# Kernel tuning notes

Measured on AMD Instinct MI355X. Metric: run time of the kernel, lower is better.

The kernel has to match this reference:

```python
import jax, jax.numpy as jnp
import numpy as np

D_MODEL = 1024
N_HEADS = 16
D_K = D_MODEL // N_HEADS
LN_EPS = 1e-5


def setup_inputs() -> dict:
    key = jax.random.key(0)
    ks = jax.random.split(key, 10)
    s = 1.0 / np.sqrt(D_MODEL)
    x = jax.random.normal(ks[0], (8, 1024, D_MODEL), dtype=jnp.float32)
    return {
        "x": x,
        "Wq": jax.random.uniform(ks[1], (D_MODEL, D_MODEL), jnp.float32, -s, s),
        "bq": jax.random.uniform(ks[2], (D_MODEL,), jnp.float32, -s, s),
        "Wk": jax.random.uniform(ks[3], (D_MODEL, D_MODEL), jnp.float32, -s, s),
        "bk": jax.random.uniform(ks[4], (D_MODEL,), jnp.float32, -s, s),
        "Wv": jax.random.uniform(ks[5], (D_MODEL, D_MODEL), jnp.float32, -s, s),
        "bv": jax.random.uniform(ks[6], (D_MODEL,), jnp.float32, -s, s),
        "Wo": jax.random.uniform(ks[7], (D_MODEL, D_MODEL), jnp.float32, -s, s),
        "bo": jax.random.uniform(ks[8], (D_MODEL,), jnp.float32, -s, s),
        "gamma": jnp.ones((D_MODEL,), jnp.float32),
        "beta": jnp.zeros((D_MODEL,), jnp.float32),
    }


def reference(x, Wq, bq, Wk, bk, Wv, bv, Wo, bo, gamma, beta):
    B, S, D = x.shape
    H, dk = N_HEADS, D_K
    # projections -> [B, H, S, dk]
    q = (x @ Wq.T + bq).reshape(B, S, H, dk).transpose(0, 2, 1, 3)
    k = (x @ Wk.T + bk).reshape(B, S, H, dk).transpose(0, 2, 1, 3)
    v = (x @ Wv.T + bv).reshape(B, S, H, dk).transpose(0, 2, 1, 3)
    scores = jnp.einsum('bhqd,bhkd->bhqk', q, k) / jnp.sqrt(jnp.float32(dk))
    attn = jax.nn.softmax(scores, axis=-1)  # dropout: eval mode (identity)
    ctx = jnp.einsum('bhqk,bhkd->bhqd', attn, v)
    ctx = ctx.transpose(0, 2, 1, 3).reshape(B, S, D)
    out = ctx @ Wo.T + bo
    h = out + x  # residual
    mu = jnp.mean(h, axis=-1, keepdims=True)
    var = jnp.mean((h - mu) ** 2, axis=-1, keepdims=True)
    y = (h - mu) * jax.lax.rsqrt(var + LN_EPS) * gamma + beta
    return y, attn
```

## Files before the change

kernel.cpp:

```cpp
#include <hip/hip_runtime.h>
#include <math.h>

#define D 1024
#define H 16
#define DK 64
#define SQ 1024
#define NB 8
#define NROW (NB*SQ)

typedef __attribute__((ext_vector_type(8))) short bf16x8;
typedef __attribute__((ext_vector_type(4))) float f32x4;

__device__ __forceinline__ ushort f2bf(float x){
    unsigned u = __builtin_bit_cast(unsigned, x);
    u += 0x7FFFu + ((u >> 16) & 1u);
    return (ushort)(u >> 16);
}
__device__ __forceinline__ float bf2f(ushort u){
    return __builtin_bit_cast(float, (unsigned)u << 16);
}

__device__ __forceinline__ f32x4 mfma16(bf16x8 a, bf16x8 b, f32x4 c){
    return __builtin_amdgcn_mfma_f32_16x16x32_bf16(a, b, c, 0, 0, 0);
}

__device__ __forceinline__ void gload16(const void* g, void* l){
    __builtin_amdgcn_global_load_lds(
        (const __attribute__((address_space(1))) unsigned int*)g,
        (__attribute__((address_space(3))) unsigned int*)l, 16, 0, 0);
}

__device__ __forceinline__ bf16x8 gld8(const ushort* p){
    return __builtin_bit_cast(bf16x8, *(const uint4*)p);
}

__global__ __launch_bounds__(256)
void cvt_all(const float* __restrict__ x,
             const float* __restrict__ Wq, const float* __restrict__ Wk,
             const float* __restrict__ Wv, const float* __restrict__ Wo,
             ushort* __restrict__ xb, ushort* __restrict__ wb_)
{
    const int bid = blockIdx.x;
    const float* s; ushort* d; size_t off;
    if (bid < 4096) { s = x; d = xb; off = (size_t)bid * 2048; }
    else {
        int r = bid - 4096;
        int wsel = r >> 9;
        if      (wsel == 0) s = Wq;
        else if (wsel == 1) s = Wk;
        else if (wsel == 2) s = Wv;
        else                s = Wo;
        d = wb_ + (size_t)wsel * 1048576;
        off = (size_t)(r & 511) * 2048;
    }
    size_t i = off + (size_t)threadIdx.x * 8;
    float4 a = *(const float4*)(s + i);
    float4 b = *(const float4*)(s + i + 4);
    ushort tmp[8] = {f2bf(a.x),f2bf(a.y),f2bf(a.z),f2bf(a.w),
                     f2bf(b.x),f2bf(b.y),f2bf(b.z),f2bf(b.w)};
    *(uint4*)(d + i) = *(uint4*)tmp;
}

__device__ __forceinline__ void stage_g(const ushort* __restrict__ g, int ldg,
                                        ushort* lds, int t)
{
#pragma unroll
    for (int i = 0; i < 2; ++i){
        int c = i*256 + t;
        int row = c >> 2, sc = c & 3;
        int gch = sc ^ (row & 3);
        gload16(g + (size_t)row*ldg + gch*8, lds + c*8);
    }
}
__device__ __forceinline__ bf16x8 gfrag(const ushort* lds, int row, int kc)
{
    uint4 v = ((const uint4*)lds)[row*4 + (kc ^ (row & 3))];
    return __builtin_bit_cast(bf16x8, v);
}

__global__ __launch_bounds__(256)
void gemm_qkv(const ushort* __restrict__ A, const ushort* __restrict__ Wp,
              const float* __restrict__ bq, const float* __restrict__ bk,
              const float* __restrict__ bv,
              ushort* __restrict__ Qb, ushort* __restrict__ Kb,
              ushort* __restrict__ Vtb)
{
    __shared__ ushort As[4096];
    __shared__ ushort Bs[4096];
    const int t = threadIdx.x, lane = t & 63, w = t >> 6;
    const int wr = w >> 1, wc = w & 1, lr = lane & 15, kg = lane >> 4;
    const int bx = blockIdx.x % 24, by = blockIdx.x / 24;
    const int i0 = by * 128, j0 = bx * 128;
    const int section = bx >> 3;
    const ushort* Ab = A  + (size_t)i0 * 1024;
    const ushort* Wb = Wp + (size_t)j0 * 1024;
    const float* bias = (section == 0) ? bq : (section == 1) ? bk : bv;
    ushort* outp      = (section == 0) ? Qb : (section == 1) ? Kb : Vtb;

    f32x4 acc[4][4];
#pragma unroll
    for (int m = 0; m < 4; ++m)
#pragma unroll
        for (int n = 0; n < 4; ++n) acc[m][n] = (f32x4){0.f,0.f,0.f,0.f};

    for (int k0 = 0; k0 < 1024; k0 += 32){
        __syncthreads();
        stage_g(Ab + k0, 1024, As, t);
        stage_g(Wb + k0, 1024, Bs, t);
        __syncthreads();
        bf16x8 af[4], bfr[4];
#pragma unroll
        for (int m = 0; m < 4; ++m) af[m]  = gfrag(As, wr*64 + m*16 + lr, kg);
#pragma unroll
        for (int n = 0; n < 4; ++n) bfr[n] = gfrag(Bs, wc*64 + n*16 + lr, kg);
#pragma unroll
        for (int m = 0; m < 4; ++m)
#pragma unroll
            for (int n = 0; n < 4; ++n)
                acc[m][n] = mfma16(af[m], bfr[n], acc[m][n]);
    }

#pragma unroll
    for (int m = 0; m < 4; ++m){
        int rt = i0 + wr*64 + m*16 + kg*4;
#pragma unroll
        for (int n = 0; n < 4; ++n){
            int jc = ((j0 + wc*64 + n*16 + lr) & 1023);
            float bj = bias[jc];
            int hh = jc >> 6, dd = jc & 63;
#pragma unroll
            for (int j = 0; j < 4; ++j){
                int i = rt + j;
                int b = i >> 10, s = i & 1023;
                float v = acc[m][n][j] + bj;
                size_t idx = (section < 2)
                    ? ((((size_t)b*H + hh)*SQ + s)*DK + dd)
                    : ((((size_t)b*H + hh)*DK + dd)*SQ + s);
                outp[idx] = f2bf(v);
            }
        }
    }
}

__global__ __launch_bounds__(256)
void gemm_o(const ushort* __restrict__ A, const ushort* __restrict__ W,
            const float* __restrict__ bias, const float* __restrict__ resid,
            float* __restrict__ out)
{
    __shared__ ushort As[4096];
    __shared__ ushort Bs[4096];
    const int t = threadIdx.x, lane = t & 63, w = t >> 6;
    const int wr = w >> 1, wc = w & 1, lr = lane & 15, kg = lane >> 4;
    const int i0 = blockIdx.y * 128, j0 = blockIdx.x * 128;
    const ushort* Ab = A + (size_t)i0 * 1024;
    const ushort* Wb = W + (size_t)j0 * 1024;

    f32x4 acc[4][4];
#pragma unroll
    for (int m = 0; m < 4; ++m)
#pragma unroll
        for (int n = 0; n < 4; ++n) acc[m][n] = (f32x4){0.f,0.f,0.f,0.f};

    for (int k0 = 0; k0 < 1024; k0 += 32){
        __syncthreads();
        stage_g(Ab + k0, 1024, As, t);
        stage_g(Wb + k0, 1024, Bs, t);
        __syncthreads();
        bf16x8 af[4], bfr[4];
#pragma unroll
        for (int m = 0; m < 4; ++m) af[m]  = gfrag(As, wr*64 + m*16 + lr, kg);
#pragma unroll
        for (int n = 0; n < 4; ++n) bfr[n] = gfrag(Bs, wc*64 + n*16 + lr, kg);
#pragma unroll
        for (int m = 0; m < 4; ++m)
#pragma unroll
            for (int n = 0; n < 4; ++n)
                acc[m][n] = mfma16(af[m], bfr[n], acc[m][n]);
    }

#pragma unroll
    for (int m = 0; m < 4; ++m){
        int rt = i0 + wr*64 + m*16 + kg*4;
#pragma unroll
        for (int n = 0; n < 4; ++n){
            int ct = j0 + wc*64 + n*16 + lr;
            float bj = bias[ct];
#pragma unroll
            for (int j = 0; j < 4; ++j){
                int i = rt + j;
                out[(size_t)i*1024 + ct] = acc[m][n][j] + bj + resid[(size_t)i*1024 + ct];
            }
        }
    }
}

__device__ __forceinline__ void stage64x64(const ushort* __restrict__ g, int ldg,
                                           ushort* lds, int t)
{
#pragma unroll
    for (int i = 0; i < 2; ++i){
        int c = i*256 + t;
        int row = c >> 3, sc = c & 7;
        int gch = sc ^ (row & 7);
        gload16(g + (size_t)row*ldg + gch*8, lds + c*8);
    }
}
__device__ __forceinline__ bf16x8 frag_ld(const ushort* lds, int row, int chunk)
{
    uint4 v = ((const uint4*)lds)[row*8 + (chunk ^ (row & 7))];
    return __builtin_bit_cast(bf16x8, v);
}

__global__ __launch_bounds__(256)
void attn_v10(const ushort* __restrict__ Q, const ushort* __restrict__ K,
              const ushort* __restrict__ Vt, float* __restrict__ attn_out,
              ushort* __restrict__ ctx)
{
    __shared__ ushort KV[2][8192];
    __shared__ ushort Ps[4][1024];

    const int t    = threadIdx.x;
    const int lane = t & 63;
    const int w    = t >> 6;
    const int lr   = lane & 15, kg = lane >> 4;
    const int bid  = blockIdx.x;
    const int qt   = bid >> 7, bh = bid & 127;
    const int b    = bh >> 4, hh = bh & 15;
    const size_t base = (size_t)bh * SQ * DK;

    bf16x8 qf[2];
    {
        const ushort* qrow = Q + base + (size_t)(qt*64 + w*16 + lr) * DK + kg*8;
        qf[0] = gld8(qrow);
        qf[1] = gld8(qrow + 32);
    }

    const float CEXP = 0.18033688011112042f;

    float lsum[4] = {0.f, 0.f, 0.f, 0.f};
    stage64x64(K + base, DK, KV[0], t);
    for (int kt = 0; kt < 16; ++kt) {
        const int cur = kt & 1;
        __syncthreads();
        if (kt < 15)
            stage64x64(K + base + (size_t)(kt+1)*64*DK, DK, KV[cur^1], t);
        const ushort* Ks = KV[cur];
#pragma unroll
        for (int n = 0; n < 4; ++n) {
            f32x4 z = {0.f,0.f,0.f,0.f};
            z = mfma16(qf[0], frag_ld(Ks, n*16+lr, kg),   z);
            z = mfma16(qf[1], frag_ld(Ks, n*16+lr, 4+kg), z);
#pragma unroll
            for (int r = 0; r < 4; ++r)
                lsum[r] += exp2f(z[r] * CEXP);
        }
    }
    float invl[4];
#pragma unroll
    for (int r = 0; r < 4; ++r) {
        float s = lsum[r];
#pragma unroll
        for (int msk = 1; msk < 16; msk <<= 1) s += __shfl_xor(s, msk, 64);
        invl[r] = 1.0f / s;
    }

    f32x4 acc_o[4];
#pragma unroll
    for (int n = 0; n < 4; ++n) acc_o[n] = (f32x4){0.f,0.f,0.f,0.f};

    float* ap0 = attn_out + ((size_t)bh*SQ + (size_t)qt*64 + w*16)*SQ;
    ushort* pw = &Ps[w][0];

    stage64x64(K  + base, DK, KV[0],        t);
    stage64x64(Vt + base, SQ, KV[0] + 4096, t);
    asm volatile("s_waitcnt vmcnt(0) lgkmcnt(0)" ::: "memory");
    __builtin_amdgcn_s_barrier();
    __builtin_amdgcn_sched_barrier(0);

    for (int kt = 0; kt < 16; ++kt) {
        const int cur = kt & 1;
        if (kt < 15) {
            stage64x64(K  + base + (size_t)(kt+1)*64*DK, DK, KV[cur^1],        t);
            stage64x64(Vt + base + (size_t)(kt+1)*64,    SQ, KV[cur^1] + 4096, t);
        }
        const ushort* Ks = KV[cur];
        const ushort* Vs = KV[cur] + 4096;

        f32x4 sc[4];
#pragma unroll
        for (int n = 0; n < 4; ++n) {
            f32x4 z = {0.f,0.f,0.f,0.f};
            z = mfma16(qf[0], frag_ld(Ks, n*16+lr, kg),   z);
            z = mfma16(qf[1], frag_ld(Ks, n*16+lr, 4+kg), z);
            sc[n] = z;
        }
#pragma unroll
        for (int n = 0; n < 4; ++n) {
#pragma unroll
            for (int r = 0; r < 4; ++r) {
                float p = exp2f(sc[n][r] * CEXP) * invl[r];
                int row = kg*4 + r, col = n*16 + lr;
                pw[row*64 + ((col>>3) ^ (row&7))*8 + (col&7)] = f2bf(p);
            }
        }
        bf16x8 a0 = frag_ld(pw, lr, kg);
        bf16x8 a1 = frag_ld(pw, lr, 4+kg);
#pragma unroll
        for (int n = 0; n < 4; ++n) {
            acc_o[n] = mfma16(a0, frag_ld(Vs, n*16+lr, kg),   acc_o[n]);
            acc_o[n] = mfma16(a1, frag_ld(Vs, n*16+lr, 4+kg), acc_o[n]);
        }
#pragma unroll
        for (int rr = 0; rr < 4; ++rr) {
            int row = kg*4 + rr;
            int cidx = row*64 + ((lr>>1) ^ (row&7))*8 + (lr&1)*4;
            uint2 pk = *(const uint2*)(pw + cidx);
            float4 o;
            o.x = bf2f((ushort)(pk.x & 0xFFFF));
            o.y = bf2f((ushort)(pk.x >> 16));
            o.z = bf2f((ushort)(pk.y & 0xFFFF));
            o.w = bf2f((ushort)(pk.y >> 16));
            *(float4*)(ap0 + (size_t)row*SQ + kt*64 + lr*4) = o;
        }
        if (kt < 15) {
            asm volatile("s_waitcnt vmcnt(4) lgkmcnt(0)" ::: "memory");
            __builtin_amdgcn_s_barrier();
            __builtin_amdgcn_sched_barrier(0);
        }
    }

    ushort* cp = ctx + ((size_t)b*SQ + (size_t)qt*64 + w*16)*D + hh*DK;
#pragma unroll
    for (int n = 0; n < 4; ++n)
#pragma unroll
        for (int r = 0; r < 4; ++r)
            cp[(size_t)(kg*4+r)*D + n*16 + lr] = f2bf(acc_o[n][r]);
}

__global__ __launch_bounds__(256)
void ln_k(const float* __restrict__ hbuf, const float* __restrict__ gamma,
          const float* __restrict__ beta, float* __restrict__ y)
{
    const int row = blockIdx.x, t = threadIdx.x;
    float4 v = ((const float4*)(hbuf + (size_t)row * D))[t];
    float s  = v.x + v.y + v.z + v.w;
    float sq = v.x*v.x + v.y*v.y + v.z*v.z + v.w*v.w;
#pragma unroll
    for (int o = 32; o >= 1; o >>= 1) {
        s  += __shfl_down(s, o, 64);
        sq += __shfl_down(sq, o, 64);
    }
    __shared__ float rs_[4], rq_[4], mu_s, rstd_s;
    int wid = t >> 6;
    if ((t & 63) == 0) { rs_[wid] = s; rq_[wid] = sq; }
    __syncthreads();
    if (t == 0) {
        float S  = rs_[0]+rs_[1]+rs_[2]+rs_[3];
        float Q2 = rq_[0]+rq_[1]+rq_[2]+rq_[3];
        float mu  = S * (1.0f/1024.0f);
        float var = Q2 * (1.0f/1024.0f) - mu*mu;
        mu_s = mu; rstd_s = rsqrtf(var + 1e-5f);
    }
    __syncthreads();
    float mu = mu_s, rstd = rstd_s;
    float4 g = ((const float4*)gamma)[t];
    float4 be = ((const float4*)beta)[t];
    float4 o;
    o.x = (v.x-mu)*rstd*g.x + be.x;
    o.y = (v.y-mu)*rstd*g.y + be.y;
    o.z = (v.z-mu)*rstd*g.z + be.z;
    o.w = (v.w-mu)*rstd*g.w + be.w;
    ((float4*)(y + (size_t)row * D))[t] = o;
}

extern "C" void kernel_launch(void* const* d_in, const int* in_sizes, int n_in,
                              void* d_out, int out_size, void* d_ws, size_t ws_size,
                              hipStream_t stream)
{
    const float* x     = (const float*)d_in[0];
    const float* Wq    = (const float*)d_in[1];
    const float* bq    = (const float*)d_in[2];
    const float* Wk    = (const float*)d_in[3];
    const float* bk    = (const float*)d_in[4];
    const float* Wv    = (const float*)d_in[5];
    const float* bv    = (const float*)d_in[6];
    const float* Wo    = (const float*)d_in[7];
    const float* bo    = (const float*)d_in[8];
    const float* gamma = (const float*)d_in[9];
    const float* beta  = (const float*)d_in[10];

    float* y    = (float*)d_out;
    float* attn = (float*)d_out + (size_t)NROW * D;

    const size_t SZ  = (size_t)NROW * D;
    const size_t WSZ = (size_t)D * D;
    ushort* ws   = (ushort*)d_ws;
    ushort* xb   = ws;
    ushort* Wpk  = xb  + SZ;
    ushort* Wob  = Wpk + 3*WSZ;
    ushort* Qb   = Wob + WSZ;
    ushort* Kb   = Qb  + SZ;
    ushort* Vtb  = Kb  + SZ;
    ushort* Cb   = Vtb + SZ;
    float*  Hb   = (float*)(Cb + SZ);

    cvt_all<<<6144, 256, 0, stream>>>(x, Wq, Wk, Wv, Wo, xb, Wpk);

    gemm_qkv<<<1536, 256, 0, stream>>>(xb, Wpk, bq, bk, bv, Qb, Kb, Vtb);

    attn_v10<<<2048, 256, 0, stream>>>(Qb, Kb, Vtb, attn, Cb);

    gemm_o<<<dim3(8, 64), 256, 0, stream>>>(Cb, Wob, bo, x, Hb);

    ln_k<<<NROW, 256, 0, stream>>>(Hb, gamma, beta, y);
}
```

Measured before the change: 334.5 us.

## Double K-tile depth in projection GEMMs and swizzle block order for L2 reuse

The QKV and output-projection GEMMs now stage 64-wide K slices instead of 32, using the 8-chunk XOR-swizzled LDS layout. This halves the number of barrier pairs per tile and puts twice as many MFMAs between syncs. Block indices are also remapped with an XCD-aware swizzle so that neighbouring tiles sharing A or W rows run on the same chiplet's L2. LDS use per block doubles, which may reduce occupancy.

```diff
diff --git a/kernel.cpp b/kernel.cpp
--- a/kernel.cpp
+++ b/kernel.cpp
@@ -32,6 +32,12 @@
 
 __device__ __forceinline__ bf16x8 gld8(const ushort* p){
     return __builtin_bit_cast(bf16x8, *(const uint4*)p);
+}
+
+__device__ __forceinline__ bf16x8 frag_ld(const ushort* lds, int row, int chunk)
+{
+    uint4 v = ((const uint4*)lds)[row*8 + (chunk ^ (row & 7))];
+    return __builtin_bit_cast(bf16x8, v);
 }
 
 __global__ __launch_bounds__(256)
@@ -61,21 +67,16 @@
     *(uint4*)(d + i) = *(uint4*)tmp;
 }
 
-__device__ __forceinline__ void stage_g(const ushort* __restrict__ g, int ldg,
-                                        ushort* lds, int t)
-{
-#pragma unroll
-    for (int i = 0; i < 2; ++i){
+__device__ __forceinline__ void stage_g64(const ushort* __restrict__ g, int ldg,
+                                          ushort* lds, int t)
+{
+#pragma unroll
+    for (int i = 0; i < 4; ++i){
         int c = i*256 + t;
-        int row = c >> 2, sc = c & 3;
-        int gch = sc ^ (row & 3);
+        int row = c >> 3, sc = c & 7;
+        int gch = sc ^ (row & 7);
         gload16(g + (size_t)row*ldg + gch*8, lds + c*8);
     }
-}
-__device__ __forceinline__ bf16x8 gfrag(const ushort* lds, int row, int kc)
-{
-    uint4 v = ((const uint4*)lds)[row*4 + (kc ^ (row & 3))];
-    return __builtin_bit_cast(bf16x8, v);
 }
 
 __global__ __launch_bounds__(256)
@@ -85,11 +86,12 @@
               ushort* __restrict__ Qb, ushort* __restrict__ Kb,
               ushort* __restrict__ Vtb)
 {
-    __shared__ ushort As[4096];
-    __shared__ ushort Bs[4096];
+    __shared__ ushort As[8192];
+    __shared__ ushort Bs[8192];
     const int t = threadIdx.x, lane = t & 63, w = t >> 6;
     const int wr = w >> 1, wc = w & 1, lr = lane & 15, kg = lane >> 4;
-    const int bx = blockIdx.x % 24, by = blockIdx.x / 24;
+    const int swz = (blockIdx.x & 7)*192 + (blockIdx.x >> 3);
+    const int bx = swz % 24, by = swz / 24;
     const int i0 = by * 128, j0 = bx * 128;
     const int section = bx >> 3;
     const ushort* Ab = A  + (size_t)i0 * 1024;
@@ -103,21 +105,24 @@
 #pragma unroll
         for (int n = 0; n < 4; ++n) acc[m][n] = (f32x4){0.f,0.f,0.f,0.f};
 
-    for (int k0 = 0; k0 < 1024; k0 += 32){
+    for (int k0 = 0; k0 < 1024; k0 += 64){
         __syncthreads();
-        stage_g(Ab + k0, 1024, As, t);
-        stage_g(Wb + k0, 1024, Bs, t);
+        stage_g64(Ab + k0, 1024, As, t);
+        stage_g64(Wb + k0, 1024, Bs, t);
         __syncthreads();
-        bf16x8 af[4], bfr[4];
-#pragma unroll
-        for (int m = 0; m < 4; ++m) af[m]  = gfrag(As, wr*64 + m*16 + lr, kg);
-#pragma unroll
-        for (int n = 0; n < 4; ++n) bfr[n] = gfrag(Bs, wc*64 + n*16 + lr, kg);
-#pragma unroll
-        for (int m = 0; m < 4; ++m)
-#pragma unroll
-            for (int n = 0; n < 4; ++n)
-                acc[m][n] = mfma16(af[m], bfr[n], acc[m][n]);
+#pragma unroll
+        for (int ks = 0; ks < 2; ++ks){
+            bf16x8 af[4], bfr[4];
+#pragma unroll
+            for (int m = 0; m < 4; ++m) af[m]  = frag_ld(As, wr*64 + m*16 + lr, ks*4 + kg);
+#pragma unroll
+            for (int n = 0; n < 4; ++n) bfr[n] = frag_ld(Bs, wc*64 + n*16 + lr, ks*4 + kg);
+#pragma unroll
+            for (int m = 0; m < 4; ++m)
+#pragma unroll
+                for (int n = 0; n < 4; ++n)
+                    acc[m][n] = mfma16(af[m], bfr[n], acc[m][n]);
+        }
     }
 
 #pragma unroll
@@ -147,11 +152,13 @@
             const float* __restrict__ bias, const float* __restrict__ resid,
             float* __restrict__ out)
 {
-    __shared__ ushort As[4096];
-    __shared__ ushort Bs[4096];
+    __shared__ ushort As[8192];
+    __shared__ ushort Bs[8192];
     const int t = threadIdx.x, lane = t & 63, w = t >> 6;
     const int wr = w >> 1, wc = w & 1, lr = lane & 15, kg = lane >> 4;
-    const int i0 = blockIdx.y * 128, j0 = blockIdx.x * 128;
+    const int swz = (blockIdx.x & 7)*64 + (blockIdx.x >> 3);
+    const int bx = swz & 7, by = swz >> 3;
+    const int i0 = by * 128, j0 = bx * 128;
     const ushort* Ab = A + (size_t)i0 * 1024;
     const ushort* Wb = W + (size_t)j0 * 1024;
 
@@ -161,21 +168,24 @@
 #pragma unroll
         for (int n = 0; n < 4; ++n) acc[m][n] = (f32x4){0.f,0.f,0.f,0.f};
 
-    for (int k0 = 0; k0 < 1024; k0 += 32){
+    for (int k0 = 0; k0 < 1024; k0 += 64){
         __syncthreads();
-        stage_g(Ab + k0, 1024, As, t);
-        stage_g(Wb + k0, 1024, Bs, t);
+        stage_g64(Ab + k0, 1024, As, t);
+        stage_g64(Wb + k0, 1024, Bs, t);
         __syncthreads();
-        bf16x8 af[4], bfr[4];
-#pragma unroll
-        for (int m = 0; m < 4; ++m) af[m]  = gfrag(As, wr*64 + m*16 + lr, kg);
-#pragma unroll
-        for (int n = 0; n < 4; ++n) bfr[n] = gfrag(Bs, wc*64 + n*16 + lr, kg);
-#pragma unroll
-        for (int m = 0; m < 4; ++m)
-#pragma unroll
-            for (int n = 0; n < 4; ++n)
-                acc[m][n] = mfma16(af[m], bfr[n], acc[m][n]);
+#pragma unroll
+        for (int ks = 0; ks < 2; ++ks){
+            bf16x8 af[4], bfr[4];
+#pragma unroll
+            for (int m = 0; m < 4; ++m) af[m]  = frag_ld(As, wr*64 + m*16 + lr, ks*4 + kg);
+#pragma unroll
+            for (int n = 0; n < 4; ++n) bfr[n] = frag_ld(Bs, wc*64 + n*16 + lr, ks*4 + kg);
+#pragma unroll
+            for (int m = 0; m < 4; ++m)
+#pragma unroll
+                for (int n = 0; n < 4; ++n)
+                    acc[m][n] = mfma16(af[m], bfr[n], acc[m][n]);
+        }
     }
 
 #pragma unroll
@@ -204,11 +214,6 @@
         int gch = sc ^ (row & 7);
         gload16(g + (size_t)row*ldg + gch*8, lds + c*8);
     }
-}
-__device__ __forceinline__ bf16x8 frag_ld(const ushort* lds, int row, int chunk)
-{
-    uint4 v = ((const uint4*)lds)[row*8 + (chunk ^ (row & 7))];
-    return __builtin_bit_cast(bf16x8, v);
 }
 
 __global__ __launch_bounds__(256)
@@ -410,7 +415,7 @@
 
     attn_v10<<<2048, 256, 0, stream>>>(Qb, Kb, Vtb, attn, Cb);
 
-    gemm_o<<<dim3(8, 64), 256, 0, stream>>>(Cb, Wob, bo, x, Hb);
+    gemm_o<<<512, 256, 0, stream>>>(Cb, Wob, bo, x, Hb);
 
     ln_k<<<NROW, 256, 0, stream>>>(Hb, gamma, beta, y);
 }
```

New measurement: 329.5 us. No clear change (-1.5%).
